# Performance work log

Hardware: AMD Instinct MI355X
Metric: run time of the kernel (lower is better)

Reference implementation:

```python
import jax, jax.numpy as jnp
import numpy as np

SEQ, D_IN, D_OUT = 4096, 1024, 1024

def setup_inputs() -> dict:
    key = jax.random.key(0)
    k1, k2, k3, k4 = jax.random.split(key, 4)
    return {
        "input": jax.random.normal(k1, (SEQ, D_IN), dtype=jnp.float32),
        "W_query": jax.random.uniform(k2, (D_IN, D_OUT), dtype=jnp.float32),
        "W_key": jax.random.uniform(k3, (D_IN, D_OUT), dtype=jnp.float32),
        "W_value": jax.random.uniform(k4, (D_IN, D_OUT), dtype=jnp.float32),
    }

def reference(input, W_query, W_key, W_value):
    # q, k, v: [S, D_out]
    q = input @ W_query
    k = input @ W_key
    v = input @ W_value
    scale = 1.0 / jnp.sqrt(jnp.asarray(k.shape[-1], dtype=q.dtype))
    scores = (q @ k.T) * scale          # [S, S]
    weights = jax.nn.softmax(scores, axis=-1)
    return weights @ v                  # [S, D_out]
```

## Files before the change

kernel.cpp:

```cpp
#include <hip/hip_runtime.h>
#include <hip/hip_bf16.h>
#include <cstdint>
#include <type_traits>


using u16 = unsigned short;
typedef __attribute__((ext_vector_type(8))) short short8;
typedef __attribute__((ext_vector_type(4))) float floatx4;
typedef __attribute__((ext_vector_type(4))) int intx4;

static constexpr int S_SEQ = 4096;
static constexpr int D_IN  = 1024;
static constexpr int D_OUT = 1024;

__device__ __forceinline__ u16 f2b(float f) {
  uint32_t u = __builtin_bit_cast(uint32_t, f);
  u = (u + 0x7FFFu + ((u >> 16) & 1u)) >> 16;
  return (u16)u;
}
__device__ __forceinline__ float b2f(u16 b) {
  return __builtin_bit_cast(float, (uint32_t)b << 16);
}
__device__ __forceinline__ void load16(const void* g, void* l) {
  __builtin_amdgcn_global_load_lds(
      (const __attribute__((address_space(1))) void*)g,
      (__attribute__((address_space(3))) void*)l,
      16, 0, 0);
}


__global__ void split_bf16_kernel(const float* __restrict__ in,
                                  u16* __restrict__ hi, u16* __restrict__ lo,
                                  int n4) {
  int i = blockIdx.x * blockDim.x + threadIdx.x;
  if (i >= n4) return;
  float4 v = reinterpret_cast<const float4*>(in)[i];
  ushort4 h, l;
  h.x = f2b(v.x); l.x = f2b(v.x - b2f(h.x));
  h.y = f2b(v.y); l.y = f2b(v.y - b2f(h.y));
  h.z = f2b(v.z); l.z = f2b(v.z - b2f(h.z));
  h.w = f2b(v.w); l.w = f2b(v.w - b2f(h.w));
  reinterpret_cast<ushort4*>(hi)[i] = h;
  reinterpret_cast<ushort4*>(lo)[i] = l;
}

__global__ void transpose_w_kernel(const float* __restrict__ Wq,
                                   const float* __restrict__ Wk,
                                   const float* __restrict__ Wv,
                                   u16* __restrict__ WtH, u16* __restrict__ WtL) {
  const int z = blockIdx.z;
  const float* src = (z == 0) ? Wq : (z == 1) ? Wk : Wv;
  u16* dH = WtH + (size_t)z * 1024 * 1024;
  u16* dL = (z < 2) ? WtL + (size_t)z * 1024 * 1024 : nullptr;
  __shared__ float tile[32][33];
  int bx = blockIdx.x * 32, by = blockIdx.y * 32;
  int tx = threadIdx.x, ty = threadIdx.y;
  for (int j = 0; j < 32; j += 8)
    tile[ty + j][tx] = src[(size_t)(by + ty + j) * 1024 + bx + tx];
  __syncthreads();
  for (int j = 0; j < 32; j += 8) {
    float v = tile[tx][ty + j];
    u16 h = f2b(v);
    size_t idx = (size_t)(bx + ty + j) * 1024 + by + tx;
    dH[idx] = h;
    if (dL) dL[idx] = f2b(v - b2f(h));
  }
}

__global__ __launch_bounds__(256)
void qkv_kernel(const u16* __restrict__ Xh, const u16* __restrict__ Xl,
                const u16* __restrict__ WtH, const u16* __restrict__ WtL,
                char* __restrict__ Qa, char* __restrict__ Qb,
                char* __restrict__ Ka, char* __restrict__ Kb,
                u16* __restrict__ Vt) {
  constexpr int BK = 32, K = D_IN;
  constexpr int TILE = 128 * BK;
  __shared__ __align__(16) u16 smem[4 * TILE];
  u16* AsH = smem;
  u16* BsH = smem + TILE;
  u16* AsL = smem + 2 * TILE;
  u16* BsL = smem + 3 * TILE;

  const int tid  = threadIdx.x;
  const int wave = tid >> 6;
  const int lane = tid & 63;
  const int bm   = blockIdx.y * 128;
  const int bn   = blockIdx.x * 128;
  const bool splitB = bn < 2048;
  const int wm   = (wave >> 1) * 64;
  const int wn   = (wave & 1) * 64;
  const int quad = lane >> 4;
  const int l16  = lane & 15;

  const int srow = wave * 16 + (lane >> 2);
  const int scol = (lane & 3) * 8;
  const size_t offA = (size_t)(bm + srow) * K + scol;
  const size_t offB = (size_t)(bn + srow) * K + scol;
  const size_t off64 = (size_t)64 * K;
  const int lds0 = wave * 512;
  const int lds1 = 2048 + wave * 512;

  floatx4 acc[4][4] = {};

  for (int k0 = 0; k0 < K; k0 += BK) {
    __syncthreads();
    load16(Xh + offA + k0,          AsH + lds0);
    load16(Xh + offA + off64 + k0,  AsH + lds1);
    load16(WtH + offB + k0,         BsH + lds0);
    load16(WtH + offB + off64 + k0, BsH + lds1);
    if (splitB) {
      load16(Xl + offA + k0,          AsL + lds0);
      load16(Xl + offA + off64 + k0,  AsL + lds1);
      load16(WtL + offB + k0,         BsL + lds0);
      load16(WtL + offB + off64 + k0, BsL + lds1);
    }
    __syncthreads();

    short8 ah[4], bh[4], al[4], bl[4];
#pragma unroll
    for (int t = 0; t < 4; ++t) {
      ah[t] = *reinterpret_cast<const short8*>(AsH + (wm + t * 16 + l16) * BK + quad * 8);
      bh[t] = *reinterpret_cast<const short8*>(BsH + (wn + t * 16 + l16) * BK + quad * 8);
    }
    if (splitB) {
#pragma unroll
      for (int t = 0; t < 4; ++t) {
        al[t] = *reinterpret_cast<const short8*>(AsL + (wm + t * 16 + l16) * BK + quad * 8);
        bl[t] = *reinterpret_cast<const short8*>(BsL + (wn + t * 16 + l16) * BK + quad * 8);
      }
    }

#pragma unroll
    for (int mt = 0; mt < 4; ++mt)
#pragma unroll
      for (int nt = 0; nt < 4; ++nt)
        acc[mt][nt] = __builtin_amdgcn_mfma_f32_16x16x32_bf16(
            ah[mt], bh[nt], acc[mt][nt], 0, 0, 0);
    if (splitB) {
#pragma unroll
      for (int mt = 0; mt < 4; ++mt)
#pragma unroll
        for (int nt = 0; nt < 4; ++nt) {
          acc[mt][nt] = __builtin_amdgcn_mfma_f32_16x16x32_bf16(
              ah[mt], bl[nt], acc[mt][nt], 0, 0, 0);
          acc[mt][nt] = __builtin_amdgcn_mfma_f32_16x16x32_bf16(
              al[mt], bh[nt], acc[mt][nt], 0, 0, 0);
        }
    }
  }

#pragma unroll
  for (int mt = 0; mt < 4; ++mt) {
#pragma unroll
    for (int nt = 0; nt < 4; ++nt) {
      const int row = bm + wm + mt * 16 + quad * 4;
      const int col = bn + wn + nt * 16 + l16;
      if (bn < 2048) {
        char* Pa = (bn < 1024) ? Qa : Ka;
        char* Pb = (bn < 1024) ? Qb : Kb;
        const int c = (bn < 1024) ? col : col - 1024;
#pragma unroll
        for (int r = 0; r < 4; ++r) {
          float v = acc[mt][nt][r];
          int q16 = (int)rintf(v * 256.f);
          q16 = min(max(q16, -32512), 32512);
          int a = (q16 + 128) >> 8;
          int b = q16 - (a << 8);
          size_t idx = (size_t)(row + r) * 1024 + c;
          Pa[idx] = (char)a;
          Pb[idx] = (char)b;
        }
      } else {
        ushort4 o;
        o.x = f2b(acc[mt][nt][0]);
        o.y = f2b(acc[mt][nt][1]);
        o.z = f2b(acc[mt][nt][2]);
        o.w = f2b(acc[mt][nt][3]);
        *reinterpret_cast<ushort4*>(Vt + (size_t)(col - 2048) * S_SEQ + row) = o;
      }
    }
  }
}

__global__ __launch_bounds__(256)
void s_i8_kernel(const char* __restrict__ Qa, const char* __restrict__ Qb,
                 const char* __restrict__ Ka, const char* __restrict__ Kb,
                 float* __restrict__ S) {
  constexpr int K = D_IN, BK = 128;
  __shared__ __align__(16) char smem[48 * 1024];
  char* QaS = smem;
  char* QbS = smem + 16384;
  char* KaS = smem + 32768;
  char* KbS = smem + 40960;

  const int tid  = threadIdx.x;
  const int wave = tid >> 6;
  const int lane = tid & 63;
  const int bm   = blockIdx.y * 128;
  const int bn   = blockIdx.x * 64;
  const int wm   = (wave >> 1) * 64;
  const int wn   = (wave & 1) * 32;
  const int quad = lane >> 4;
  const int l16  = lane & 15;

  const int srow = lane >> 3;
  const int scol = ((lane & 7) ^ srow) * 16;
  int gQ[4], gK[2];
#pragma unroll
  for (int j = 0; j < 4; ++j)
    gQ[j] = (bm + j * 32 + wave * 8 + srow) * K + scol;
#pragma unroll
  for (int j = 0; j < 2; ++j)
    gK[j] = (bn + j * 32 + wave * 8 + srow) * K + scol;
  const int lQ[4] = {(0 * 32 + wave * 8) * 128, (1 * 32 + wave * 8) * 128,
                     (2 * 32 + wave * 8) * 128, (3 * 32 + wave * 8) * 128};
  const int lK[2] = {(0 * 32 + wave * 8) * 128, (1 * 32 + wave * 8) * 128};

  const int r7 = l16 & 7;
  int cA[4], cB[2];
#pragma unroll
  for (int t = 0; t < 4; ++t)
    cA[t] = (wm + t * 16 + l16) * 128 + ((quad ^ r7) * 16);
#pragma unroll
  for (int t = 0; t < 2; ++t)
    cB[t] = (wn + t * 16 + l16) * 128 + ((quad ^ r7) * 16);

  intx4 accH[4][2] = {};
  intx4 accM[4][2] = {};
  intx4 accL[4][2] = {};

  for (int k0 = 0; k0 < K; k0 += BK) {
    __syncthreads();
#pragma unroll
    for (int j = 0; j < 4; ++j) {
      load16(Qa + gQ[j] + k0, QaS + lQ[j]);
      load16(Qb + gQ[j] + k0, QbS + lQ[j]);
    }
#pragma unroll
    for (int j = 0; j < 2; ++j) {
      load16(Ka + gK[j] + k0, KaS + lK[j]);
      load16(Kb + gK[j] + k0, KbS + lK[j]);
    }
    __syncthreads();

#pragma unroll
    for (int s = 0; s < 2; ++s) {
      const int so = s * 64;
      intx4 ah[4], al[4];
#pragma unroll
      for (int t = 0; t < 4; ++t) {
        ah[t] = *reinterpret_cast<const intx4*>(QaS + (cA[t] ^ so));
        al[t] = *reinterpret_cast<const intx4*>(QbS + (cA[t] ^ so));
      }
#pragma unroll
      for (int nt = 0; nt < 2; ++nt) {
        intx4 bh = *reinterpret_cast<const intx4*>(KaS + (cB[nt] ^ so));
#pragma unroll
        for (int mt = 0; mt < 4; ++mt) {
          accH[mt][nt] = __builtin_amdgcn_mfma_i32_16x16x64_i8(ah[mt], bh, accH[mt][nt], 0, 0, 0);
          accM[mt][nt] = __builtin_amdgcn_mfma_i32_16x16x64_i8(al[mt], bh, accM[mt][nt], 0, 0, 0);
        }
        intx4 bl = *reinterpret_cast<const intx4*>(KbS + (cB[nt] ^ so));
#pragma unroll
        for (int mt = 0; mt < 4; ++mt) {
          accM[mt][nt] = __builtin_amdgcn_mfma_i32_16x16x64_i8(ah[mt], bl, accM[mt][nt], 0, 0, 0);
          accL[mt][nt] = __builtin_amdgcn_mfma_i32_16x16x64_i8(al[mt], bl, accL[mt][nt], 0, 0, 0);
        }
      }
    }
  }

  constexpr float SC = 4.76837158203125e-07f;
#pragma unroll
  for (int mt = 0; mt < 4; ++mt)
#pragma unroll
    for (int nt = 0; nt < 2; ++nt) {
      const int row = bm + wm + mt * 16 + quad * 4;
      const int col = bn + wn + nt * 16 + l16;
#pragma unroll
      for (int r = 0; r < 4; ++r) {
        long long fix = (((long long)accH[mt][nt][r]) << 16) +
                        (((long long)accM[mt][nt][r]) << 8) +
                        (long long)accL[mt][nt][r];
        S[(size_t)(row + r) * S_SEQ + col] = (float)fix * SC;
      }
    }
}

__global__ __launch_bounds__(256)
void pv_kernel(const u16* __restrict__ P, const u16* __restrict__ Vt,
               float* __restrict__ Osl) {
  constexpr int LDA = S_SEQ;
  constexpr int KS  = S_SEQ / 4;
  constexpr int BK  = 128;
  __shared__ __align__(16) u16 smem[2 * 128 * 128];
  u16* As = smem;
  u16* Bs = smem + 128 * 128;

  const int tid  = threadIdx.x;
  const int wave = tid >> 6;
  const int lane = tid & 63;
  const int bn   = blockIdx.x * 128;
  const int bm   = blockIdx.y * 128;
  const int kz   = blockIdx.z * KS;
  const int wm   = (wave >> 1) * 64;
  const int wn   = (wave & 1) * 64;
  const int quad = lane >> 4;
  const int l16  = lane & 15;

  const int srow = lane >> 4;
  const int r7s  = 4 * (wave & 1) + srow;
  const int gcol = ((lane & 15) ^ r7s) * 8;
  int gA[8], gB[8], lb[8];
#pragma unroll
  for (int j = 0; j < 8; ++j) {
    const int row = j * 16 + wave * 4;
    gA[j] = (bm + row + srow) * LDA + kz + gcol;
    gB[j] = (bn + row + srow) * LDA + kz + gcol;
    lb[j] = row * 128;
  }

  int baseA[4], baseB[4], r7A[4], r7B[4];
#pragma unroll
  for (int t = 0; t < 4; ++t) {
    const int Ra = wm + t * 16 + l16;
    const int Rb = wn + t * 16 + l16;
    baseA[t] = Ra * 128; r7A[t] = Ra & 7;
    baseB[t] = Rb * 128; r7B[t] = Rb & 7;
  }

  floatx4 acc[4][4] = {};

  for (int k0 = 0; k0 < KS; k0 += BK) {
    __syncthreads();
#pragma unroll
    for (int j = 0; j < 8; ++j) {
      load16(P + gA[j] + k0,  As + lb[j]);
      load16(Vt + gB[j] + k0, Bs + lb[j]);
    }
    __syncthreads();

#pragma unroll
    for (int s = 0; s < 4; ++s) {
      short8 af[4], bf[4];
#pragma unroll
      for (int t = 0; t < 4; ++t) {
        af[t] = *reinterpret_cast<const short8*>(
            As + baseA[t] + (((4 * s + quad) ^ r7A[t]) * 8));
        bf[t] = *reinterpret_cast<const short8*>(
            Bs + baseB[t] + (((4 * s + quad) ^ r7B[t]) * 8));
      }
#pragma unroll
      for (int mt = 0; mt < 4; ++mt)
#pragma unroll
        for (int nt = 0; nt < 4; ++nt)
          acc[mt][nt] = __builtin_amdgcn_mfma_f32_16x16x32_bf16(
              af[mt], bf[nt], acc[mt][nt], 0, 0, 0);
    }
  }

  float* C = Osl + (size_t)blockIdx.z * S_SEQ * D_OUT;
#pragma unroll
  for (int mt = 0; mt < 4; ++mt)
#pragma unroll
    for (int nt = 0; nt < 4; ++nt) {
      const int row = bm + wm + mt * 16 + quad * 4;
      const int col = bn + wn + nt * 16 + l16;
#pragma unroll
      for (int r = 0; r < 4; ++r)
        C[(size_t)(row + r) * D_OUT + col] = acc[mt][nt][r];
    }
}

__global__ void add4_kernel(const float* __restrict__ s,
                            float* __restrict__ o, int n4) {
  int i = blockIdx.x * blockDim.x + threadIdx.x;
  if (i >= n4) return;
  const float4* s4 = reinterpret_cast<const float4*>(s);
  float4 x = s4[i];
  float4 y = s4[i + n4];
  float4 z = s4[i + 2 * n4];
  float4 w = s4[i + 3 * n4];
  x.x += y.x + z.x + w.x;
  x.y += y.y + z.y + w.y;
  x.z += y.z + z.z + w.z;
  x.w += y.w + z.w + w.w;
  reinterpret_cast<float4*>(o)[i] = x;
}

__global__ __launch_bounds__(256)
void softmax_kernel(const float* __restrict__ S, u16* __restrict__ P) {
  const int row = blockIdx.x, tid = threadIdx.x;
  const int lane = tid & 63, wave = tid >> 6;
  __shared__ float red[4];
  const float4* src = reinterpret_cast<const float4*>(S + (size_t)row * S_SEQ);
  ushort4* dst = reinterpret_cast<ushort4*>(P + (size_t)row * S_SEQ);

  float4 v[4];
  float m = -INFINITY;
#pragma unroll
  for (int t = 0; t < 4; ++t) {
    v[t] = src[tid + t * 256];
    m = fmaxf(m, fmaxf(fmaxf(v[t].x, v[t].y), fmaxf(v[t].z, v[t].w)));
  }
#pragma unroll
  for (int off = 1; off < 64; off <<= 1) m = fmaxf(m, __shfl_xor(m, off));
  if (lane == 0) red[wave] = m;
  __syncthreads();
  m = fmaxf(fmaxf(red[0], red[1]), fmaxf(red[2], red[3]));

  float e[16];
  float l = 0.f;
#pragma unroll
  for (int t = 0; t < 4; ++t) {
    e[4 * t + 0] = __expf(v[t].x - m);
    e[4 * t + 1] = __expf(v[t].y - m);
    e[4 * t + 2] = __expf(v[t].z - m);
    e[4 * t + 3] = __expf(v[t].w - m);
    l += e[4 * t + 0] + e[4 * t + 1] + e[4 * t + 2] + e[4 * t + 3];
  }
#pragma unroll
  for (int off = 1; off < 64; off <<= 1) l += __shfl_xor(l, off);
  __syncthreads();
  if (lane == 0) red[wave] = l;
  __syncthreads();
  const float li = 1.f / (red[0] + red[1] + red[2] + red[3]);

#pragma unroll
  for (int t = 0; t < 4; ++t) {
    ushort4 o;
    o.x = f2b(e[4 * t + 0] * li);
    o.y = f2b(e[4 * t + 1] * li);
    o.z = f2b(e[4 * t + 2] * li);
    o.w = f2b(e[4 * t + 3] * li);
    dst[tid + t * 256] = o;
  }
}


extern "C" void kernel_launch(void* const* d_in, const int* in_sizes, int n_in,
                              void* d_out, int out_size, void* d_ws, size_t ws_size,
                              hipStream_t stream) {
  const float* X  = (const float*)d_in[0];
  const float* Wq = (const float*)d_in[1];
  const float* Wk = (const float*)d_in[2];
  const float* Wv = (const float*)d_in[3];
  float* O = (float*)d_out;
  char* ws = (char*)d_ws;

  const size_t MB = 1u << 20;
  u16*   Xh  = (u16*)(ws);
  u16*   Xl  = (u16*)(ws + 8 * MB);
  u16*   WtH = (u16*)(ws + 16 * MB);
  u16*   WtL = (u16*)(ws + 22 * MB);
  u16*   P   = (u16*)(ws);
  char*  Qa  = (char*)(ws + 32 * MB);
  char*  Qb  = (char*)(ws + 36 * MB);
  char*  Ka  = (char*)(ws + 40 * MB);
  char*  Kb  = (char*)(ws + 44 * MB);
  u16*   Vt  = (u16*)(ws + 64 * MB);
  float* Ss  = (float*)(ws + 72 * MB);
  float* Osl = (float*)(ws + 72 * MB);

  split_bf16_kernel<<<(S_SEQ * D_IN / 4 + 255) / 256, 256, 0, stream>>>(
      X, Xh, Xl, S_SEQ * D_IN / 4);
  transpose_w_kernel<<<dim3(32, 32, 3), dim3(32, 8), 0, stream>>>(
      Wq, Wk, Wv, WtH, WtL);

  qkv_kernel<<<dim3(3072 / 128, S_SEQ / 128), 256, 0, stream>>>(
      Xh, Xl, WtH, WtL, Qa, Qb, Ka, Kb, Vt);

  s_i8_kernel<<<dim3(S_SEQ / 64, S_SEQ / 128), 256, 0, stream>>>(
      Qa, Qb, Ka, Kb, Ss);

  softmax_kernel<<<S_SEQ, 256, 0, stream>>>(Ss, P);

  pv_kernel<<<dim3(D_OUT / 128, S_SEQ / 128, 4), 256, 0, stream>>>(P, Vt, Osl);
  add4_kernel<<<(S_SEQ * D_OUT / 4 + 255) / 256, 256, 0, stream>>>(
      Osl, O, S_SEQ * D_OUT / 4);
}
```

Baseline: 277.7 us.

## Merge input conversion kernels, halve PV split-K, store partials as bf16

Fuses the X split and the weight transpose/convert into one launch, using a fourth z-slice for the X conversion and early-exiting the unused weight blocks. The PV split-K factor drops from 4 to 2, and partial outputs are stored as bf16 instead of fp32. The final reduction then reads two bf16 partials instead of four fp32 ones. This cuts a launch and much of the partial-sum traffic, but rounding the partials to bf16 costs precision and fewer split-K slices lowers parallelism in pv_kernel.

```diff
diff --git a/kernel.cpp b/kernel.cpp
--- a/kernel.cpp
+++ b/kernel.cpp
@@ -28,33 +28,33 @@
       16, 0, 0);
 }
 
-
-__global__ void split_bf16_kernel(const float* __restrict__ in,
-                                  u16* __restrict__ hi, u16* __restrict__ lo,
-                                  int n4) {
-  int i = blockIdx.x * blockDim.x + threadIdx.x;
-  if (i >= n4) return;
-  float4 v = reinterpret_cast<const float4*>(in)[i];
-  ushort4 h, l;
-  h.x = f2b(v.x); l.x = f2b(v.x - b2f(h.x));
-  h.y = f2b(v.y); l.y = f2b(v.y - b2f(h.y));
-  h.z = f2b(v.z); l.z = f2b(v.z - b2f(h.z));
-  h.w = f2b(v.w); l.w = f2b(v.w - b2f(h.w));
-  reinterpret_cast<ushort4*>(hi)[i] = h;
-  reinterpret_cast<ushort4*>(lo)[i] = l;
-}
-
-__global__ void transpose_w_kernel(const float* __restrict__ Wq,
-                                   const float* __restrict__ Wk,
-                                   const float* __restrict__ Wv,
-                                   u16* __restrict__ WtH, u16* __restrict__ WtL) {
+__global__ void convert_kernel(const float* __restrict__ X,
+                               const float* __restrict__ Wq,
+                               const float* __restrict__ Wk,
+                               const float* __restrict__ Wv,
+                               u16* __restrict__ Xh, u16* __restrict__ Xl,
+                               u16* __restrict__ WtH, u16* __restrict__ WtL) {
   const int z = blockIdx.z;
+  const int tx = threadIdx.x, ty = threadIdx.y;
+  if (z == 3) {
+    const int bid = blockIdx.y * 128 + blockIdx.x;
+    const int i = bid * 256 + ty * 32 + tx;
+    float4 v = reinterpret_cast<const float4*>(X)[i];
+    ushort4 h, l;
+    h.x = f2b(v.x); l.x = f2b(v.x - b2f(h.x));
+    h.y = f2b(v.y); l.y = f2b(v.y - b2f(h.y));
+    h.z = f2b(v.z); l.z = f2b(v.z - b2f(h.z));
+    h.w = f2b(v.w); l.w = f2b(v.w - b2f(h.w));
+    reinterpret_cast<ushort4*>(Xh)[i] = h;
+    reinterpret_cast<ushort4*>(Xl)[i] = l;
+    return;
+  }
+  if (blockIdx.x >= 32) return;
   const float* src = (z == 0) ? Wq : (z == 1) ? Wk : Wv;
   u16* dH = WtH + (size_t)z * 1024 * 1024;
   u16* dL = (z < 2) ? WtL + (size_t)z * 1024 * 1024 : nullptr;
   __shared__ float tile[32][33];
   int bx = blockIdx.x * 32, by = blockIdx.y * 32;
-  int tx = threadIdx.x, ty = threadIdx.y;
   for (int j = 0; j < 32; j += 8)
     tile[ty + j][tx] = src[(size_t)(by + ty + j) * 1024 + bx + tx];
   __syncthreads();
@@ -289,9 +289,9 @@
 
 __global__ __launch_bounds__(256)
 void pv_kernel(const u16* __restrict__ P, const u16* __restrict__ Vt,
-               float* __restrict__ Osl) {
+               u16* __restrict__ Osl) {
   constexpr int LDA = S_SEQ;
-  constexpr int KS  = S_SEQ / 4;
+  constexpr int KS  = S_SEQ / 2;
   constexpr int BK  = 128;
   __shared__ __align__(16) u16 smem[2 * 128 * 128];
   u16* As = smem;
@@ -359,7 +359,7 @@
     }
   }
 
-  float* C = Osl + (size_t)blockIdx.z * S_SEQ * D_OUT;
+  u16* C = Osl + (size_t)blockIdx.z * S_SEQ * D_OUT;
 #pragma unroll
   for (int mt = 0; mt < 4; ++mt)
 #pragma unroll
@@ -368,23 +368,21 @@
       const int col = bn + wn + nt * 16 + l16;
 #pragma unroll
       for (int r = 0; r < 4; ++r)
-        C[(size_t)(row + r) * D_OUT + col] = acc[mt][nt][r];
-    }
-}
-
-__global__ void add4_kernel(const float* __restrict__ s,
+        C[(size_t)(row + r) * D_OUT + col] = f2b(acc[mt][nt][r]);
+    }
+}
+
+__global__ void add2_kernel(const u16* __restrict__ s,
                             float* __restrict__ o, int n4) {
   int i = blockIdx.x * blockDim.x + threadIdx.x;
   if (i >= n4) return;
-  const float4* s4 = reinterpret_cast<const float4*>(s);
-  float4 x = s4[i];
-  float4 y = s4[i + n4];
-  float4 z = s4[i + 2 * n4];
-  float4 w = s4[i + 3 * n4];
-  x.x += y.x + z.x + w.x;
-  x.y += y.y + z.y + w.y;
-  x.z += y.z + z.z + w.z;
-  x.w += y.w + z.w + w.w;
+  ushort4 a = reinterpret_cast<const ushort4*>(s)[i];
+  ushort4 b = reinterpret_cast<const ushort4*>(s)[i + n4];
+  float4 x;
+  x.x = b2f(a.x) + b2f(b.x);
+  x.y = b2f(a.y) + b2f(b.y);
+  x.z = b2f(a.z) + b2f(b.z);
+  x.w = b2f(a.w) + b2f(b.w);
   reinterpret_cast<float4*>(o)[i] = x;
 }
 
@@ -460,12 +458,10 @@
   char*  Kb  = (char*)(ws + 44 * MB);
   u16*   Vt  = (u16*)(ws + 64 * MB);
   float* Ss  = (float*)(ws + 72 * MB);
-  float* Osl = (float*)(ws + 72 * MB);
-
-  split_bf16_kernel<<<(S_SEQ * D_IN / 4 + 255) / 256, 256, 0, stream>>>(
-      X, Xh, Xl, S_SEQ * D_IN / 4);
-  transpose_w_kernel<<<dim3(32, 32, 3), dim3(32, 8), 0, stream>>>(
-      Wq, Wk, Wv, WtH, WtL);
+  u16*   Osl = (u16*)(ws + 72 * MB);
+
+  convert_kernel<<<dim3(128, 32, 4), dim3(32, 8), 0, stream>>>(
+      X, Wq, Wk, Wv, Xh, Xl, WtH, WtL);
 
   qkv_kernel<<<dim3(3072 / 128, S_SEQ / 128), 256, 0, stream>>>(
       Xh, Xl, WtH, WtL, Qa, Qb, Ka, Kb, Vt);
@@ -475,7 +471,7 @@
 
   softmax_kernel<<<S_SEQ, 256, 0, stream>>>(Ss, P);
 
-  pv_kernel<<<dim3(D_OUT / 128, S_SEQ / 128, 4), 256, 0, stream>>>(P, Vt, Osl);
-  add4_kernel<<<(S_SEQ * D_OUT / 4 + 255) / 256, 256, 0, stream>>>(
+  pv_kernel<<<dim3(D_OUT / 128, S_SEQ / 128, 2), 256, 0, stream>>>(P, Vt, Osl);
+  add2_kernel<<<(S_SEQ * D_OUT / 4 + 255) / 256, 256, 0, stream>>>(
       Osl, O, S_SEQ * D_OUT / 4);
 }
```

New measurement: 270.2 us. 1.03x faster.
